# Kernel optimization log

Measured on AMD Instinct MI355X. Metric: run time of the kernel, lower is better.

Reference implementation:

```python
import jax, jax.numpy as jnp
import numpy as np

E, H, I, T = 8, 2048, 1024, 16384  # experts, hidden, moe_intermediate, total tokens


def setup_inputs() -> dict:
    key = jax.random.key(0)
    k1, k2, k3, k4 = jax.random.split(key, 4)
    hidden_states = jax.random.normal(k1, (T, H), dtype=jnp.float32)
    # ragged per-expert token counts, summing exactly to T (tokens pre-sorted by expert)
    group_sizes = jnp.array([1024, 3072, 2048, 4096, 512, 1536, 2560, 1536], dtype=jnp.int32)
    std = 0.01  # nn.initializers.normal() default stddev
    gate_w = jax.random.normal(k2, (E, H, I), dtype=jnp.float32) * std
    up_w = jax.random.normal(k3, (E, H, I), dtype=jnp.float32) * std
    down_w = jax.random.normal(k4, (E, I, H), dtype=jnp.float32) * std
    return {"hidden_states": hidden_states, "gate_w": gate_w, "up_w": up_w,
            "down_w": down_w, "group_sizes": group_sizes}


def reference(hidden_states, gate_w, up_w, down_w, group_sizes):
    # grouped GEMM: rows of hidden_states are contiguous per-expert blocks of
    # sizes group_sizes[e]; each block is multiplied by that expert's kernel.
    g = jax.lax.ragged_dot(hidden_states, gate_w, group_sizes)   # [T, I]
    u = jax.lax.ragged_dot(hidden_states, up_w, group_sizes)     # [T, I]
    h = jax.nn.silu(g) * u                                       # SwiGLU gating
    return jax.lax.ragged_dot(h, down_w, group_sizes)            # [T, H]
```

## Files before the change

### kernel.cpp

```cpp
#include <hip/hip_runtime.h>
#include <hip/hip_bf16.h>

#define E_ 8
#define H_ 2048
#define I_ 1024
#define T_ 16384
#define BM 128
#define BN 128
#define BK 32
#define MAX_MT 136

typedef __bf16 bf16x8 __attribute__((ext_vector_type(8)));
typedef float f32x4 __attribute__((ext_vector_type(4)));

__device__ __forceinline__ unsigned short f2bf(float f) {
  unsigned int x = __float_as_uint(f);
  x += 0x7FFFu + ((x >> 16) & 1u);
  return (unsigned short)(x >> 16);
}

__device__ __forceinline__ void gl_lds16(const void* g, void* s) {
  __builtin_amdgcn_global_load_lds(
      (const __attribute__((address_space(1))) void*)g,
      (__attribute__((address_space(3))) void*)s, 16, 0, 0);
}

__device__ __forceinline__ bool find_tile(const int* gs, int tile, int& e,
                                          int& row0, int& rowEnd) {
  int base = 0, tb = 0;
  e = -1;
  for (int i = 0; i < E_; i++) {
    int g = gs[i];
    int nt = (g + BM - 1) >> 7;
    if (e < 0 && tile < tb + nt) {
      e = i;
      row0 = base + (tile - tb) * BM;
      rowEnd = base + g;
    }
    tb += nt;
    base += g;
  }
  return e >= 0;
}


__global__ void cvt_hs(const float* __restrict__ in, ushort* __restrict__ out) {
  size_t i = ((size_t)blockIdx.x * 256 + threadIdx.x) * 8;
  float4 a = *(const float4*)(in + i);
  float4 b = *(const float4*)(in + i + 4);
  union { ushort u[8]; uint4 v; } p;
  p.u[0] = f2bf(a.x); p.u[1] = f2bf(a.y); p.u[2] = f2bf(a.z); p.u[3] = f2bf(a.w);
  p.u[4] = f2bf(b.x); p.u[5] = f2bf(b.y); p.u[6] = f2bf(b.z); p.u[7] = f2bf(b.w);
  *(uint4*)(out + i) = p.v;
}

__global__ void cvt_tr(const float* __restrict__ in, ushort* __restrict__ out,
                       int K, int N) {
  __shared__ ushort tile[64][65];
  int n0 = blockIdx.x * 64, k0 = blockIdx.y * 64;
  const float* src = in + (size_t)blockIdx.z * K * N;
  ushort* dst = out + (size_t)blockIdx.z * K * N;
  int t = threadIdx.x;
  int rb = t >> 4, c4 = (t & 15) * 4;
#pragma unroll
  for (int i = 0; i < 4; i++) {
    int r = rb + i * 16;
    float4 v = *(const float4*)(src + (size_t)(k0 + r) * N + n0 + c4);
    tile[r][c4 + 0] = f2bf(v.x);
    tile[r][c4 + 1] = f2bf(v.y);
    tile[r][c4 + 2] = f2bf(v.z);
    tile[r][c4 + 3] = f2bf(v.w);
  }
  __syncthreads();
#pragma unroll
  for (int i = 0; i < 2; i++) {
    int c = t + i * 256;
    int n = c >> 3, kc = c & 7;
    union { ushort u[8]; uint4 v; } p;
#pragma unroll
    for (int j = 0; j < 8; j++) p.u[j] = tile[kc * 8 + j][n];
    *(uint4*)(dst + (size_t)(n0 + n) * K + k0 + kc * 8) = p.v;
  }
}

__global__ __launch_bounds__(256, 2) void gemm_gateup(
    const ushort* __restrict__ A, const ushort* __restrict__ BgT,
    const ushort* __restrict__ BuT, const int* __restrict__ gs,
    ushort* __restrict__ Hb) {
  __shared__ __align__(16) ushort sA[BM * BK];
  __shared__ __align__(16) ushort sG[BN * BK];
  __shared__ __align__(16) ushort sU[BN * BK];

  int e, row0, rowEnd;
  if (!find_tile(gs, blockIdx.x, e, row0, rowEnd)) return;
  const int n0 = blockIdx.y * BN;

  const int t = threadIdx.x;
  const int lane = t & 63;
  const int w = t >> 6;
  const int wm = w & 1, wn = w >> 1;

  const int c0 = t, c1 = t + 256;
  const int r0 = c0 >> 2, kc0 = c0 & 3;
  const int r1 = c1 >> 2, kc1 = c1 & 3;
  int ar0 = row0 + r0; if (ar0 > T_ - 1) ar0 = T_ - 1;
  int ar1 = row0 + r1; if (ar1 > T_ - 1) ar1 = T_ - 1;

  const ushort* pa0 = A + (size_t)ar0 * H_ + kc0 * 8;
  const ushort* pa1 = A + (size_t)ar1 * H_ + kc1 * 8;
  const ushort* bgb = BgT + ((size_t)e * I_ + n0) * H_;
  const ushort* bub = BuT + ((size_t)e * I_ + n0) * H_;
  const ushort* pg0 = bgb + (size_t)r0 * H_ + kc0 * 8;
  const ushort* pg1 = bgb + (size_t)r1 * H_ + kc1 * 8;
  const ushort* pu0 = bub + (size_t)r0 * H_ + kc0 * 8;
  const ushort* pu1 = bub + (size_t)r1 * H_ + kc1 * 8;

  ushort* dA0 = &sA[w * 512]; ushort* dA1 = &sA[2048 + w * 512];
  ushort* dG0 = &sG[w * 512]; ushort* dG1 = &sG[2048 + w * 512];
  ushort* dU0 = &sU[w * 512]; ushort* dU1 = &sU[2048 + w * 512];

  const int koff = (lane >> 4) * 8;
  const ushort* aF = &sA[(wm * 64 + (lane & 15)) * BK + koff];
  const ushort* gF = &sG[(wn * 64 + (lane & 15)) * BK + koff];
  const ushort* uF = &sU[(wn * 64 + (lane & 15)) * BK + koff];

  f32x4 accG[4][4], accU[4][4];
#pragma unroll
  for (int mi = 0; mi < 4; mi++)
#pragma unroll
    for (int ni = 0; ni < 4; ni++) {
      accG[mi][ni] = (f32x4){0.f, 0.f, 0.f, 0.f};
      accU[mi][ni] = (f32x4){0.f, 0.f, 0.f, 0.f};
    }

  for (int k0 = 0; k0 < H_; k0 += BK) {
    gl_lds16(pa0, dA0); gl_lds16(pa1, dA1);
    gl_lds16(pg0, dG0); gl_lds16(pg1, dG1);
    gl_lds16(pu0, dU0); gl_lds16(pu1, dU1);
    pa0 += BK; pa1 += BK; pg0 += BK; pg1 += BK; pu0 += BK; pu1 += BK;
    __syncthreads();

    bf16x8 af[4], gf[4], uf[4];
#pragma unroll
    for (int i = 0; i < 4; i++) {
      af[i] = *(const bf16x8*)(aF + i * 16 * BK);
      gf[i] = *(const bf16x8*)(gF + i * 16 * BK);
      uf[i] = *(const bf16x8*)(uF + i * 16 * BK);
    }
#pragma unroll
    for (int mi = 0; mi < 4; mi++)
#pragma unroll
      for (int ni = 0; ni < 4; ni++) {
        accG[mi][ni] = __builtin_amdgcn_mfma_f32_16x16x32_bf16(af[mi], gf[ni], accG[mi][ni], 0, 0, 0);
        accU[mi][ni] = __builtin_amdgcn_mfma_f32_16x16x32_bf16(af[mi], uf[ni], accU[mi][ni], 0, 0, 0);
      }
    __syncthreads();
  }

  const int crow = row0 + wm * 64 + ((lane >> 4) << 2);
  const int ccol = n0 + wn * 64 + (lane & 15);
#pragma unroll
  for (int mi = 0; mi < 4; mi++)
#pragma unroll
    for (int ni = 0; ni < 4; ni++)
#pragma unroll
      for (int r = 0; r < 4; r++) {
        int row = crow + mi * 16 + r;
        if (row < rowEnd) {
          float g = accG[mi][ni][r];
          float u = accU[mi][ni][r];
          float h = (g / (1.0f + __expf(-g))) * u;
          Hb[(size_t)row * I_ + ccol + ni * 16] = f2bf(h);
        }
      }
}

__global__ __launch_bounds__(256, 2) void gemm_down(
    const ushort* __restrict__ A, const ushort* __restrict__ BdT,
    const int* __restrict__ gs, float* __restrict__ Out) {
  __shared__ __align__(16) ushort sA[BM * BK];
  __shared__ __align__(16) ushort sB[BN * BK];

  int e, row0, rowEnd;
  if (!find_tile(gs, blockIdx.x, e, row0, rowEnd)) return;
  const int n0 = blockIdx.y * BN;

  const int t = threadIdx.x;
  const int lane = t & 63;
  const int w = t >> 6;
  const int wm = w & 1, wn = w >> 1;

  const int c0 = t, c1 = t + 256;
  const int r0 = c0 >> 2, kc0 = c0 & 3;
  const int r1 = c1 >> 2, kc1 = c1 & 3;
  int ar0 = row0 + r0; if (ar0 > T_ - 1) ar0 = T_ - 1;
  int ar1 = row0 + r1; if (ar1 > T_ - 1) ar1 = T_ - 1;

  const ushort* pa0 = A + (size_t)ar0 * I_ + kc0 * 8;
  const ushort* pa1 = A + (size_t)ar1 * I_ + kc1 * 8;
  const ushort* bb = BdT + ((size_t)e * H_ + n0) * I_;
  const ushort* pb0 = bb + (size_t)r0 * I_ + kc0 * 8;
  const ushort* pb1 = bb + (size_t)r1 * I_ + kc1 * 8;

  ushort* dA0 = &sA[w * 512]; ushort* dA1 = &sA[2048 + w * 512];
  ushort* dB0 = &sB[w * 512]; ushort* dB1 = &sB[2048 + w * 512];

  const int koff = (lane >> 4) * 8;
  const ushort* aF = &sA[(wm * 64 + (lane & 15)) * BK + koff];
  const ushort* bF = &sB[(wn * 64 + (lane & 15)) * BK + koff];

  f32x4 acc[4][4];
#pragma unroll
  for (int mi = 0; mi < 4; mi++)
#pragma unroll
    for (int ni = 0; ni < 4; ni++) acc[mi][ni] = (f32x4){0.f, 0.f, 0.f, 0.f};

  for (int k0 = 0; k0 < I_; k0 += BK) {
    gl_lds16(pa0, dA0); gl_lds16(pa1, dA1);
    gl_lds16(pb0, dB0); gl_lds16(pb1, dB1);
    pa0 += BK; pa1 += BK; pb0 += BK; pb1 += BK;
    __syncthreads();

    bf16x8 af[4], bf[4];
#pragma unroll
    for (int i = 0; i < 4; i++) {
      af[i] = *(const bf16x8*)(aF + i * 16 * BK);
      bf[i] = *(const bf16x8*)(bF + i * 16 * BK);
    }
#pragma unroll
    for (int mi = 0; mi < 4; mi++)
#pragma unroll
      for (int ni = 0; ni < 4; ni++)
        acc[mi][ni] = __builtin_amdgcn_mfma_f32_16x16x32_bf16(af[mi], bf[ni], acc[mi][ni], 0, 0, 0);
    __syncthreads();
  }

  const int crow = row0 + wm * 64 + ((lane >> 4) << 2);
  const int ccol = n0 + wn * 64 + (lane & 15);
#pragma unroll
  for (int mi = 0; mi < 4; mi++)
#pragma unroll
    for (int ni = 0; ni < 4; ni++)
#pragma unroll
      for (int r = 0; r < 4; r++) {
        int row = crow + mi * 16 + r;
        if (row < rowEnd) Out[(size_t)row * H_ + ccol + ni * 16] = acc[mi][ni][r];
      }
}

extern "C" void kernel_launch(void* const* d_in, const int* in_sizes, int n_in,
                              void* d_out, int out_size, void* d_ws, size_t ws_size,
                              hipStream_t stream) {
  const float* hs = (const float*)d_in[0];
  const float* gw = (const float*)d_in[1];
  const float* uw = (const float*)d_in[2];
  const float* dw = (const float*)d_in[3];
  const int* gs = (const int*)d_in[4];
  float* out = (float*)d_out;

  ushort* hsb = (ushort*)d_ws;
  ushort* wgT = hsb + (size_t)T_ * H_;
  ushort* wuT = wgT + (size_t)E_ * H_ * I_;
  ushort* wdT = wuT + (size_t)E_ * H_ * I_;
  ushort* hb  = wdT + (size_t)E_ * H_ * I_;

  cvt_hs<<<((size_t)T_ * H_) / (256 * 8), 256, 0, stream>>>(hs, hsb);
  cvt_tr<<<dim3(I_ / 64, H_ / 64, E_), 256, 0, stream>>>(gw, wgT, H_, I_);
  cvt_tr<<<dim3(I_ / 64, H_ / 64, E_), 256, 0, stream>>>(uw, wuT, H_, I_);
  cvt_tr<<<dim3(H_ / 64, I_ / 64, E_), 256, 0, stream>>>(dw, wdT, I_, H_);

  gemm_gateup<<<dim3(MAX_MT, I_ / BN), 256, 0, stream>>>(hsb, wgT, wuT, gs, hb);
  gemm_down<<<dim3(MAX_MT, H_ / BN), 256, 0, stream>>>(hb, wdT, gs, out);
}
```

Baseline: 654.0 us.

## Double K tile to 64 with XOR-swizzled LDS layout and explicit waitcnt sync

```diff
diff --git a/kernel.cpp b/kernel.cpp
--- a/kernel.cpp
+++ b/kernel.cpp
@@ -7,7 +7,7 @@
 #define T_ 16384
 #define BM 128
 #define BN 128
-#define BK 32
+#define BK 64
 #define MAX_MT 136
 
 typedef __bf16 bf16x8 __attribute__((ext_vector_type(8)));
@@ -23,6 +23,11 @@
   __builtin_amdgcn_global_load_lds(
       (const __attribute__((address_space(1))) void*)g,
       (__attribute__((address_space(3))) void*)s, 16, 0, 0);
+}
+
+__device__ __forceinline__ void sync_full() {
+  __builtin_amdgcn_s_waitcnt(0);
+  __syncthreads();
 }
 
 __device__ __forceinline__ bool find_tile(const int* gs, int tile, int& e,
@@ -100,29 +105,31 @@
   const int w = t >> 6;
   const int wm = w & 1, wn = w >> 1;
 
-  const int c0 = t, c1 = t + 256;
-  const int r0 = c0 >> 2, kc0 = c0 & 3;
-  const int r1 = c1 >> 2, kc1 = c1 & 3;
-  int ar0 = row0 + r0; if (ar0 > T_ - 1) ar0 = T_ - 1;
-  int ar1 = row0 + r1; if (ar1 > T_ - 1) ar1 = T_ - 1;
-
-  const ushort* pa0 = A + (size_t)ar0 * H_ + kc0 * 8;
-  const ushort* pa1 = A + (size_t)ar1 * H_ + kc1 * 8;
-  const ushort* bgb = BgT + ((size_t)e * I_ + n0) * H_;
-  const ushort* bub = BuT + ((size_t)e * I_ + n0) * H_;
-  const ushort* pg0 = bgb + (size_t)r0 * H_ + kc0 * 8;
-  const ushort* pg1 = bgb + (size_t)r1 * H_ + kc1 * 8;
-  const ushort* pu0 = bub + (size_t)r0 * H_ + kc0 * 8;
-  const ushort* pu1 = bub + (size_t)r1 * H_ + kc1 * 8;
-
-  ushort* dA0 = &sA[w * 512]; ushort* dA1 = &sA[2048 + w * 512];
-  ushort* dG0 = &sG[w * 512]; ushort* dG1 = &sG[2048 + w * 512];
-  ushort* dU0 = &sU[w * 512]; ushort* dU1 = &sU[2048 + w * 512];
-
-  const int koff = (lane >> 4) * 8;
-  const ushort* aF = &sA[(wm * 64 + (lane & 15)) * BK + koff];
-  const ushort* gF = &sG[(wn * 64 + (lane & 15)) * BK + koff];
-  const ushort* uF = &sU[(wn * 64 + (lane & 15)) * BK + koff];
+  int offAB[4];
+  int offA[4];
+#pragma unroll
+  for (int i = 0; i < 4; i++) {
+    int c = i * 256 + t;
+    int r = c >> 3;
+    int kcs = (c & 7) ^ (r & 7);
+    offAB[i] = r * H_ + kcs * 8;
+    int ar = row0 + r; if (ar > T_ - 1) ar = T_ - 1;
+    offA[i] = ar * H_ + kcs * 8;
+  }
+  const ushort* pA = A;
+  const ushort* pG = BgT + ((size_t)e * I_ + n0) * H_;
+  const ushort* pU = BuT + ((size_t)e * I_ + n0) * H_;
+  const int ldst = w * 64 * 8;
+
+  const int l15 = lane & 15, l7 = lane & 7, lk = lane >> 4;
+  const int sw0 = (lk ^ l7) * 8;
+  const int sw1 = ((lk + 4) ^ l7) * 8;
+  const ushort* aF0 = sA + (wm * 64 + l15) * BK + sw0;
+  const ushort* aF1 = sA + (wm * 64 + l15) * BK + sw1;
+  const ushort* gF0 = sG + (wn * 64 + l15) * BK + sw0;
+  const ushort* gF1 = sG + (wn * 64 + l15) * BK + sw1;
+  const ushort* uF0 = sU + (wn * 64 + l15) * BK + sw0;
+  const ushort* uF1 = sU + (wn * 64 + l15) * BK + sw1;
 
   f32x4 accG[4][4], accU[4][4];
 #pragma unroll
@@ -134,27 +141,33 @@
     }
 
   for (int k0 = 0; k0 < H_; k0 += BK) {
-    gl_lds16(pa0, dA0); gl_lds16(pa1, dA1);
-    gl_lds16(pg0, dG0); gl_lds16(pg1, dG1);
-    gl_lds16(pu0, dU0); gl_lds16(pu1, dU1);
-    pa0 += BK; pa1 += BK; pg0 += BK; pg1 += BK; pu0 += BK; pu1 += BK;
-    __syncthreads();
-
-    bf16x8 af[4], gf[4], uf[4];
 #pragma unroll
     for (int i = 0; i < 4; i++) {
-      af[i] = *(const bf16x8*)(aF + i * 16 * BK);
-      gf[i] = *(const bf16x8*)(gF + i * 16 * BK);
-      uf[i] = *(const bf16x8*)(uF + i * 16 * BK);
-    }
-#pragma unroll
-    for (int mi = 0; mi < 4; mi++)
-#pragma unroll
-      for (int ni = 0; ni < 4; ni++) {
-        accG[mi][ni] = __builtin_amdgcn_mfma_f32_16x16x32_bf16(af[mi], gf[ni], accG[mi][ni], 0, 0, 0);
-        accU[mi][ni] = __builtin_amdgcn_mfma_f32_16x16x32_bf16(af[mi], uf[ni], accU[mi][ni], 0, 0, 0);
-      }
-    __syncthreads();
+      gl_lds16(pA + offA[i],  sA + i * 2048 + ldst);
+      gl_lds16(pG + offAB[i], sG + i * 2048 + ldst);
+      gl_lds16(pU + offAB[i], sU + i * 2048 + ldst);
+    }
+    pA += BK; pG += BK; pU += BK;
+    sync_full();
+
+#pragma unroll
+    for (int ks = 0; ks < 2; ks++) {
+      bf16x8 af[4], gf[4], uf[4];
+#pragma unroll
+      for (int i = 0; i < 4; i++) {
+        af[i] = *(const bf16x8*)((ks ? aF1 : aF0) + i * 16 * BK);
+        gf[i] = *(const bf16x8*)((ks ? gF1 : gF0) + i * 16 * BK);
+        uf[i] = *(const bf16x8*)((ks ? uF1 : uF0) + i * 16 * BK);
+      }
+#pragma unroll
+      for (int mi = 0; mi < 4; mi++)
+#pragma unroll
+        for (int ni = 0; ni < 4; ni++) {
+          accG[mi][ni] = __builtin_amdgcn_mfma_f32_16x16x32_bf16(af[mi], gf[ni], accG[mi][ni], 0, 0, 0);
+          accU[mi][ni] = __builtin_amdgcn_mfma_f32_16x16x32_bf16(af[mi], uf[ni], accU[mi][ni], 0, 0, 0);
+        }
+    }
+    sync_full();
   }
 
   const int crow = row0 + wm * 64 + ((lane >> 4) << 2);
@@ -175,7 +188,7 @@
       }
 }
 
-__global__ __launch_bounds__(256, 2) void gemm_down(
+__global__ __launch_bounds__(256, 3) void gemm_down(
     const ushort* __restrict__ A, const ushort* __restrict__ BdT,
     const int* __restrict__ gs, float* __restrict__ Out) {
   __shared__ __align__(16) ushort sA[BM * BK];
@@ -190,24 +203,27 @@
   const int w = t >> 6;
   const int wm = w & 1, wn = w >> 1;
 
-  const int c0 = t, c1 = t + 256;
-  const int r0 = c0 >> 2, kc0 = c0 & 3;
-  const int r1 = c1 >> 2, kc1 = c1 & 3;
-  int ar0 = row0 + r0; if (ar0 > T_ - 1) ar0 = T_ - 1;
-  int ar1 = row0 + r1; if (ar1 > T_ - 1) ar1 = T_ - 1;
-
-  const ushort* pa0 = A + (size_t)ar0 * I_ + kc0 * 8;
-  const ushort* pa1 = A + (size_t)ar1 * I_ + kc1 * 8;
-  const ushort* bb = BdT + ((size_t)e * H_ + n0) * I_;
-  const ushort* pb0 = bb + (size_t)r0 * I_ + kc0 * 8;
-  const ushort* pb1 = bb + (size_t)r1 * I_ + kc1 * 8;
-
-  ushort* dA0 = &sA[w * 512]; ushort* dA1 = &sA[2048 + w * 512];
-  ushort* dB0 = &sB[w * 512]; ushort* dB1 = &sB[2048 + w * 512];
-
-  const int koff = (lane >> 4) * 8;
-  const ushort* aF = &sA[(wm * 64 + (lane & 15)) * BK + koff];
-  const ushort* bF = &sB[(wn * 64 + (lane & 15)) * BK + koff];
+  int offB[4], offA[4];
+#pragma unroll
+  for (int i = 0; i < 4; i++) {
+    int c = i * 256 + t;
+    int r = c >> 3;
+    int kcs = (c & 7) ^ (r & 7);
+    offB[i] = r * I_ + kcs * 8;
+    int ar = row0 + r; if (ar > T_ - 1) ar = T_ - 1;
+    offA[i] = ar * I_ + kcs * 8;
+  }
+  const ushort* pA = A;
+  const ushort* pB = BdT + ((size_t)e * H_ + n0) * I_;
+  const int ldst = w * 64 * 8;
+
+  const int l15 = lane & 15, l7 = lane & 7, lk = lane >> 4;
+  const int sw0 = (lk ^ l7) * 8;
+  const int sw1 = ((lk + 4) ^ l7) * 8;
+  const ushort* aF0 = sA + (wm * 64 + l15) * BK + sw0;
+  const ushort* aF1 = sA + (wm * 64 + l15) * BK + sw1;
+  const ushort* bF0 = sB + (wn * 64 + l15) * BK + sw0;
+  const ushort* bF1 = sB + (wn * 64 + l15) * BK + sw1;
 
   f32x4 acc[4][4];
 #pragma unroll
@@ -216,23 +232,29 @@
     for (int ni = 0; ni < 4; ni++) acc[mi][ni] = (f32x4){0.f, 0.f, 0.f, 0.f};
 
   for (int k0 = 0; k0 < I_; k0 += BK) {
-    gl_lds16(pa0, dA0); gl_lds16(pa1, dA1);
-    gl_lds16(pb0, dB0); gl_lds16(pb1, dB1);
-    pa0 += BK; pa1 += BK; pb0 += BK; pb1 += BK;
-    __syncthreads();
-
-    bf16x8 af[4], bf[4];
 #pragma unroll
     for (int i = 0; i < 4; i++) {
-      af[i] = *(const bf16x8*)(aF + i * 16 * BK);
-      bf[i] = *(const bf16x8*)(bF + i * 16 * BK);
-    }
-#pragma unroll
-    for (int mi = 0; mi < 4; mi++)
-#pragma unroll
-      for (int ni = 0; ni < 4; ni++)
-        acc[mi][ni] = __builtin_amdgcn_mfma_f32_16x16x32_bf16(af[mi], bf[ni], acc[mi][ni], 0, 0, 0);
-    __syncthreads();
+      gl_lds16(pA + offA[i], sA + i * 2048 + ldst);
+      gl_lds16(pB + offB[i], sB + i * 2048 + ldst);
+    }
+    pA += BK; pB += BK;
+    sync_full();
+
+#pragma unroll
+    for (int ks = 0; ks < 2; ks++) {
+      bf16x8 af[4], bf[4];
+#pragma unroll
+      for (int i = 0; i < 4; i++) {
+        af[i] = *(const bf16x8*)((ks ? aF1 : aF0) + i * 16 * BK);
+        bf[i] = *(const bf16x8*)((ks ? bF1 : bF0) + i * 16 * BK);
+      }
+#pragma unroll
+      for (int mi = 0; mi < 4; mi++)
+#pragma unroll
+        for (int ni = 0; ni < 4; ni++)
+          acc[mi][ni] = __builtin_amdgcn_mfma_f32_16x16x32_bf16(af[mi], bf[ni], acc[mi][ni], 0, 0, 0);
+    }
+    sync_full();
   }
 
   const int crow = row0 + wm * 64 + ((lane >> 4) << 2);
```

After: 600.4 us. 8.2% less time.
